# Performance work log

Measured on AMD Instinct MI355X. Metric: run time of the kernel, lower is better.

Reference implementation:

```python
import jax, jax.numpy as jnp
import numpy as np

FACTOR = 5

def setup_inputs() -> dict:
    key = jax.random.key(0)
    k1, k2, k3, k4 = jax.random.split(key, 4)
    B, L, H, D = 4, 2048, 8, 64
    sample_k = min(FACTOR * int(np.ceil(np.log(L))), L)  # 40
    return {
        "queries": jax.random.normal(k1, (B, L, H, D), dtype=jnp.float32),
        "keys": jax.random.normal(k2, (B, L, H, D), dtype=jnp.float32),
        "values": jax.random.normal(k3, (B, L, H, D), dtype=jnp.float32),
        "index_sample": jax.random.randint(k4, (L, sample_k), 0, L, dtype=jnp.int32),
    }

def reference(queries, keys, values, index_sample):
    # [B, L, H, D] -> [B, H, L, D]
    Q = jnp.transpose(queries, (0, 2, 1, 3))
    K = jnp.transpose(keys, (0, 2, 1, 3))
    V = jnp.transpose(values, (0, 2, 1, 3))
    B, H, L_Q, D = Q.shape
    L_K = K.shape[2]
    u = min(FACTOR * int(np.ceil(np.log(L_Q))), L_Q)  # n_top

    # --- _prob_QK: sampled QK scores ---
    # K_sample: [B, H, L_Q, sample_k, D]
    K_sample = K[:, :, index_sample, :]
    # Q_K_sample[b,h,l,s] = Q[b,h,l,:] . K_sample[b,h,l,s,:]
    Q_K_sample = jnp.einsum('bhld,bhlsd->bhls', Q, K_sample)
    # sparsity measure M: max - mean over L_K
    M = Q_K_sample.max(axis=-1) - Q_K_sample.sum(axis=-1) / L_K  # [B,H,L_Q]
    _, M_top = jax.lax.top_k(M, u)  # [B,H,u]

    # reduced Q -> full scores against all keys
    Q_reduce = jnp.take_along_axis(Q, M_top[..., None], axis=2)  # [B,H,u,D]
    scores = jnp.einsum('bhud,bhkd->bhuk', Q_reduce, K)  # [B,H,u,L_K]
    scale = 1.0 / jnp.sqrt(jnp.asarray(D, dtype=scores.dtype))
    scores = scores * scale

    # --- initial context: mean of V over keys (mask_flag=False) ---
    V_mean = V.mean(axis=-2)  # [B,H,D]
    context = jnp.broadcast_to(V_mean[:, :, None, :], (B, H, L_Q, D))

    # --- update context at top-u query positions ---
    attn = jax.nn.softmax(scores, axis=-1)  # [B,H,u,L_K]
    ctx_top = jnp.einsum('bhuk,bhkd->bhud', attn, V)  # [B,H,u,D]
    b_idx = jnp.arange(B)[:, None, None]
    h_idx = jnp.arange(H)[None, :, None]
    context = context.at[b_idx, h_idx, M_top].set(ctx_top)
    return context  # [B, H, L_Q, D]
```

## Files before the change

### kernel.cpp

```cpp
#include <hip/hip_runtime.h>
#include <math.h>

#define LL 2048
#define HH 8
#define DD 64
#define SK 40
#define UU 40
#define SCALE 0.125f


__global__ __launch_bounds__(512) void k_m(
    const float* __restrict__ Q, const float* __restrict__ K,
    const int* __restrict__ idxs, float* __restrict__ Mout)
{
  int bx = blockIdx.x;
  int xcd = bx & 7, slot = bx >> 3;
  int b = xcd >> 1;
  int l = ((xcd & 1) << 10) | slot;
  int t = threadIdx.x;
  int h = t >> 6, lane = t & 63;
  int sg = lane >> 2, dg = lane & 3;

  int kb = b << 20;
  int qoff = kb + (l << 9) + (h << 6) + (dg << 2);
  float4 qv[4];
#pragma unroll
  for (int i = 0; i < 4; ++i)
    qv[i] = *(const float4*)(Q + qoff + i * 16);

  const int* ip = idxs + l * SK;
  int kconst = kb + (h << 6) + (dg << 2);
  float mx = -INFINITY, sum = 0.f;

#pragma unroll
  for (int c = 0; c < 3; ++c) {
    int s = c * 16 + sg;
    float p = 0.f;
    if (s < SK) {
      int koff = kconst + (ip[s] << 9);
      const float* krow = K + koff;
#pragma unroll
      for (int i = 0; i < 4; ++i) {
        float4 kv = *(const float4*)(krow + i * 16);
        p += qv[i].x * kv.x + qv[i].y * kv.y + qv[i].z * kv.z + qv[i].w * kv.w;
      }
    }
    p += __shfl_xor(p, 1);
    p += __shfl_xor(p, 2);
    if (s < SK) { mx = fmaxf(mx, p); sum += p; }
  }
#pragma unroll
  for (int off = 4; off <= 32; off <<= 1) {
    mx = fmaxf(mx, __shfl_xor(mx, off));
    sum += __shfl_xor(sum, off);
  }
  if (lane == 0) Mout[((b * HH + h) << 11) + l] = mx - sum * (1.0f / (float)LL);
}

__global__ __launch_bounds__(256) void k_topk(
    const float* __restrict__ Mv, int* __restrict__ Mtop)
{
  __shared__ float sv[LL];
  __shared__ float wm[4];
  __shared__ int wi[4];
  int bh = blockIdx.x;
  int t = threadIdx.x, w = t >> 6, ln = t & 63;
  for (int i = t; i < LL; i += 256) sv[i] = Mv[bh * LL + i];
  __syncthreads();
  for (int r = 0; r < UU; ++r) {
    float bv = -INFINITY; int bi = 0;
#pragma unroll
    for (int j = 0; j < 8; ++j) {
      int i = t + (j << 8);
      float v = sv[i];
      if (v > bv) { bv = v; bi = i; }
    }
#pragma unroll
    for (int off = 1; off < 64; off <<= 1) {
      float ov = __shfl_xor(bv, off);
      int oi = __shfl_xor(bi, off);
      if (ov > bv || (ov == bv && oi < bi)) { bv = ov; bi = oi; }
    }
    if (ln == 0) { wm[w] = bv; wi[w] = bi; }
    __syncthreads();
    if (t == 0) {
      float Bv = wm[0]; int Bi = wi[0];
#pragma unroll
      for (int k = 1; k < 4; ++k)
        if (wm[k] > Bv || (wm[k] == Bv && wi[k] < Bi)) { Bv = wm[k]; Bi = wi[k]; }
      Mtop[bh * UU + r] = Bi;
      sv[Bi] = -INFINITY;
    }
    __syncthreads();
  }
}

__global__ __launch_bounds__(256) void k_vpart(
    const float* __restrict__ V, float* __restrict__ part)
{
  int blk = blockIdx.x;
  int bh = blk >> 3, c = blk & 7;
  int b = bh >> 3, h = bh & 7;
  int t = threadIdx.x, d = t & 63, w = t >> 6;
  int l0 = (c << 8) + (w << 6);
  int base = (b << 20) + (l0 << 9) + (h << 6) + d;
  float a0 = 0, a1 = 0, a2 = 0, a3 = 0;
  for (int j = 0; j < 64; j += 4) {
    a0 += V[base + ((j + 0) << 9)];
    a1 += V[base + ((j + 1) << 9)];
    a2 += V[base + ((j + 2) << 9)];
    a3 += V[base + ((j + 3) << 9)];
  }
  __shared__ float sm[4][64];
  sm[w][d] = a0 + a1 + a2 + a3;
  __syncthreads();
  if (t < 64) part[(blk << 6) + t] = sm[0][t] + sm[1][t] + sm[2][t] + sm[3][t];
}

__global__ __launch_bounds__(256) void k_fill(
    const float4* __restrict__ part4, float4* __restrict__ out4)
{
  int i = blockIdx.x * 256 + threadIdx.x;
  int bh = i >> 15;
  __shared__ float4 vm[16];
  if (threadIdx.x < 16) {
    int d4 = threadIdx.x;
    float4 s = {0, 0, 0, 0};
#pragma unroll
    for (int c = 0; c < 8; ++c) {
      float4 p = part4[((bh << 3) + c) * 16 + d4];
      s.x += p.x; s.y += p.y; s.z += p.z; s.w += p.w;
    }
    const float inv = 1.0f / (float)LL;
    s.x *= inv; s.y *= inv; s.z *= inv; s.w *= inv;
    vm[d4] = s;
  }
  __syncthreads();
  out4[i] = vm[i & 15];
}

__global__ __launch_bounds__(512) void k_attn2(
    const float* __restrict__ Q, const float* __restrict__ K,
    const float* __restrict__ V, const int* __restrict__ Mtop,
    float* __restrict__ pm, float* __restrict__ pl, float4* __restrict__ pO4)
{
  __shared__ float4 Ks4[1024];
  __shared__ float Ps[8][256];
  __shared__ float4 Os4[4][2][4][16];
  __shared__ int gqi[8];

  int bx = blockIdx.x;
  int ch = bx & 7;
  int slot = bx >> 3;
  int bh = slot / 5, rg = slot % 5;
  int b = bh >> 3, h = bh & 7;
  int t = threadIdx.x;
  int w = t >> 6, ln = t & 63;
  int l0 = ch << 8;

  if (t < 8) gqi[t] = Mtop[bh * UU + rg * 8 + t];
  __syncthreads();

  float4 qv[16];
  {
    const float4* qrow = (const float4*)Q + (((b << 11) + gqi[w]) << 7) + (h << 4);
#pragma unroll
    for (int i = 0; i < 16; ++i) qv[i] = qrow[i];
  }

  const float4* K4 = (const float4*)K;
  int kbase = (((b << 11) + l0) << 7) + (h << 4);
  int col0 = t >> 4, d40 = t & 15;
  int sw0 = col0 * 16 + (d40 ^ (col0 & 7));
  float4 g0 = K4[kbase + col0 * 128 + d40];
  float4 g1 = K4[kbase + (col0 + 32) * 128 + d40];

  float sc[4];
#pragma unroll
  for (int st = 0; st < 4; ++st) {
    __syncthreads();
    Ks4[sw0] = g0;
    Ks4[sw0 + 512] = g1;
    float4 n0, n1;
    if (st < 3) {
      int lr = (st + 1) * 64;
      n0 = K4[kbase + (lr + col0) * 128 + d40];
      n1 = K4[kbase + (lr + col0 + 32) * 128 + d40];
    }
    __syncthreads();
    float s = 0.f;
#pragma unroll
    for (int d4 = 0; d4 < 16; ++d4) {
      float4 kv = Ks4[ln * 16 + (d4 ^ (ln & 7))];
      s += qv[d4].x * kv.x + qv[d4].y * kv.y + qv[d4].z * kv.z + qv[d4].w * kv.w;
    }
    sc[st] = s * SCALE;
    g0 = n0; g1 = n1;
  }

  float m = fmaxf(fmaxf(sc[0], sc[1]), fmaxf(sc[2], sc[3]));
#pragma unroll
  for (int off = 1; off < 64; off <<= 1) m = fmaxf(m, __shfl_xor(m, off));
  float lsum = 0.f;
#pragma unroll
  for (int st = 0; st < 4; ++st) {
    float p = __expf(sc[st] - m);
    Ps[w][st * 64 + ln] = p;
    lsum += p;
  }
#pragma unroll
  for (int off = 1; off < 64; off <<= 1) lsum += __shfl_xor(lsum, off);
  if (ln == 0) {
    int prow = bh * UU + rg * 8 + w;
    pm[prow * 8 + ch] = m;
    pl[prow * 8 + ch] = lsum;
  }
  __syncthreads();

  int rw = w >> 2, cq = w & 3;
  int cg = ln >> 4, d4 = ln & 15;
  float4 o0 = {0,0,0,0}, o1 = {0,0,0,0}, o2 = {0,0,0,0}, o3 = {0,0,0,0};
  int vb = (((b << 11) + l0 + cq * 64) << 7) + (h << 4);
  const float4* V4 = (const float4*)V;
#pragma unroll
  for (int i = 0; i < 16; ++i) {
    int c = i * 4 + cg;
    float4 v4 = V4[vb + c * 128 + d4];
    float p0 = Ps[rw * 4 + 0][cq * 64 + c];
    float p1 = Ps[rw * 4 + 1][cq * 64 + c];
    float p2 = Ps[rw * 4 + 2][cq * 64 + c];
    float p3 = Ps[rw * 4 + 3][cq * 64 + c];
    o0.x += p0 * v4.x; o0.y += p0 * v4.y; o0.z += p0 * v4.z; o0.w += p0 * v4.w;
    o1.x += p1 * v4.x; o1.y += p1 * v4.y; o1.z += p1 * v4.z; o1.w += p1 * v4.w;
    o2.x += p2 * v4.x; o2.y += p2 * v4.y; o2.z += p2 * v4.z; o2.w += p2 * v4.w;
    o3.x += p3 * v4.x; o3.y += p3 * v4.y; o3.z += p3 * v4.z; o3.w += p3 * v4.w;
  }
#pragma unroll
  for (int off = 16; off <= 32; off <<= 1) {
    o0.x += __shfl_xor(o0.x, off); o0.y += __shfl_xor(o0.y, off);
    o0.z += __shfl_xor(o0.z, off); o0.w += __shfl_xor(o0.w, off);
    o1.x += __shfl_xor(o1.x, off); o1.y += __shfl_xor(o1.y, off);
    o1.z += __shfl_xor(o1.z, off); o1.w += __shfl_xor(o1.w, off);
    o2.x += __shfl_xor(o2.x, off); o2.y += __shfl_xor(o2.y, off);
    o2.z += __shfl_xor(o2.z, off); o2.w += __shfl_xor(o2.w, off);
    o3.x += __shfl_xor(o3.x, off); o3.y += __shfl_xor(o3.y, off);
    o3.z += __shfl_xor(o3.z, off); o3.w += __shfl_xor(o3.w, off);
  }
  if (cg == 0) {
    Os4[cq][rw][0][d4] = o0;
    Os4[cq][rw][1][d4] = o1;
    Os4[cq][rw][2][d4] = o2;
    Os4[cq][rw][3][d4] = o3;
  }
  __syncthreads();

  if (t < 128) {
    int r = t >> 4, dd = t & 15;
    float4 a = Os4[0][r >> 2][r & 3][dd];
    float4 bq = Os4[1][r >> 2][r & 3][dd];
    float4 cc = Os4[2][r >> 2][r & 3][dd];
    float4 dq = Os4[3][r >> 2][r & 3][dd];
    float4 s;
    s.x = a.x + bq.x + cc.x + dq.x;
    s.y = a.y + bq.y + cc.y + dq.y;
    s.z = a.z + bq.z + cc.z + dq.z;
    s.w = a.w + bq.w + cc.w + dq.w;
    int prow = bh * UU + rg * 8 + r;
    pO4[(prow * 8 + ch) * 16 + dd] = s;
  }
}

__global__ __launch_bounds__(256) void k_comb(
    const float* __restrict__ pm, const float* __restrict__ pl,
    const float* __restrict__ pO, const int* __restrict__ Mtop,
    float* __restrict__ out)
{
  int row = blockIdx.x * 4 + (threadIdx.x >> 6);
  int ln = threadIdx.x & 63;
  int bh = row / UU, r40 = row % UU;
  float mm[8];
#pragma unroll
  for (int c = 0; c < 8; ++c) mm[c] = pm[row * 8 + c];
  float ms = mm[0];
#pragma unroll
  for (int c = 1; c < 8; ++c) ms = fmaxf(ms, mm[c]);
  float wsum = 0.f, o = 0.f;
#pragma unroll
  for (int c = 0; c < 8; ++c) {
    float wc = __expf(mm[c] - ms);
    wsum += wc * pl[row * 8 + c];
    o += wc * pO[(row * 8 + c) * 64 + ln];
  }
  int gq = Mtop[bh * UU + r40];
  out[((bh * LL + gq) << 6) + ln] = o / wsum;
}

extern "C" void kernel_launch(void* const* d_in, const int* in_sizes, int n_in,
                              void* d_out, int out_size, void* d_ws, size_t ws_size,
                              hipStream_t stream)
{
  (void)in_sizes; (void)n_in; (void)out_size; (void)ws_size;
  const float* Q = (const float*)d_in[0];
  const float* K = (const float*)d_in[1];
  const float* V = (const float*)d_in[2];
  const int* idxs = (const int*)d_in[3];
  float* out = (float*)d_out;

  float* wsf = (float*)d_ws;
  float* M     = wsf;
  float* part  = wsf + 65536;
  int*   Mtop  = (int*)(wsf + 83968);
  float* pm    = wsf + 85248;
  float* pl    = wsf + 95488;
  float* pO    = wsf + 105728;

  k_m    <<<8192, 512, 0, stream>>>(Q, K, idxs, M);
  k_topk <<<32,   256, 0, stream>>>(M, Mtop);
  k_vpart<<<256,  256, 0, stream>>>(V, part);
  k_fill <<<4096, 256, 0, stream>>>((const float4*)part, (float4*)out);
  k_attn2<<<1280, 512, 0, stream>>>(Q, K, V, Mtop, pm, pl, (float4*)pO);
  k_comb <<<320,  256, 0, stream>>>(pm, pl, pO, Mtop, out);
}
```

Baseline: 215.7 us.

## Restructure sampled-QK kernel: one wave per query row, all heads per wave

The sparsity-measure kernel now gives each block 8 query rows, one per wavefront, with each wave covering all 8 heads using 8 lanes per head. The row's sample indices are staged in shared memory, and 8 key gathers are issued before any compute to expose more memory-level parallelism. Each gathered key row (all heads, 2KB) is read contiguously by a single wave, and the grid shrinks eightfold. This trades fewer blocks and extra register pressure for better coalescing and less index reloading.

```diff
diff --git a/kernel.cpp b/kernel.cpp
--- a/kernel.cpp
+++ b/kernel.cpp
@@ -9,52 +9,55 @@
 #define SCALE 0.125f
 
 
-__global__ __launch_bounds__(512) void k_m(
+__global__ __launch_bounds__(512, 4) void k_m(
     const float* __restrict__ Q, const float* __restrict__ K,
     const int* __restrict__ idxs, float* __restrict__ Mout)
 {
+  __shared__ int sidx[8 * SK];
   int bx = blockIdx.x;
   int xcd = bx & 7, slot = bx >> 3;
   int b = xcd >> 1;
-  int l = ((xcd & 1) << 10) | slot;
+  int l0 = ((xcd & 1) << 10) | (slot << 3);
   int t = threadIdx.x;
-  int h = t >> 6, lane = t & 63;
-  int sg = lane >> 2, dg = lane & 3;
-
-  int kb = b << 20;
-  int qoff = kb + (l << 9) + (h << 6) + (dg << 2);
-  float4 qv[4];
-#pragma unroll
-  for (int i = 0; i < 4; ++i)
-    qv[i] = *(const float4*)(Q + qoff + i * 16);
-
-  const int* ip = idxs + l * SK;
-  int kconst = kb + (h << 6) + (dg << 2);
+  int w = t >> 6, lane = t & 63;
+  int l = l0 + w;
+  int h = lane >> 3, dg = lane & 7;
+
+  if (t < 8 * SK) sidx[t] = idxs[l0 * SK + t];
+
+  const float4* Q4 = (const float4*)Q;
+  int qoff = (((b << 11) + l) << 7) + (h << 4) + (dg << 1);
+  float4 q0 = Q4[qoff], q1 = Q4[qoff + 1];
+
+  const float4* K4 = (const float4*)K;
+  int kbb = b << 18;
+  int klo = (h << 4) + (dg << 1);
+
+  __syncthreads();
+
   float mx = -INFINITY, sum = 0.f;
-
-#pragma unroll
-  for (int c = 0; c < 3; ++c) {
-    int s = c * 16 + sg;
-    float p = 0.f;
-    if (s < SK) {
-      int koff = kconst + (ip[s] << 9);
-      const float* krow = K + koff;
-#pragma unroll
-      for (int i = 0; i < 4; ++i) {
-        float4 kv = *(const float4*)(krow + i * 16);
-        p += qv[i].x * kv.x + qv[i].y * kv.y + qv[i].z * kv.z + qv[i].w * kv.w;
-      }
-    }
-    p += __shfl_xor(p, 1);
-    p += __shfl_xor(p, 2);
-    if (s < SK) { mx = fmaxf(mx, p); sum += p; }
-  }
-#pragma unroll
-  for (int off = 4; off <= 32; off <<= 1) {
-    mx = fmaxf(mx, __shfl_xor(mx, off));
-    sum += __shfl_xor(sum, off);
-  }
-  if (lane == 0) Mout[((b * HH + h) << 11) + l] = mx - sum * (1.0f / (float)LL);
+#pragma unroll
+  for (int s0 = 0; s0 < SK; s0 += 8) {
+    float4 ka[8], kc[8];
+#pragma unroll
+    for (int j = 0; j < 8; ++j) {
+      int idx = sidx[w * SK + s0 + j];
+      int off = kbb + (idx << 7) + klo;
+      ka[j] = K4[off];
+      kc[j] = K4[off + 1];
+    }
+#pragma unroll
+    for (int j = 0; j < 8; ++j) {
+      float p = q0.x * ka[j].x + q0.y * ka[j].y + q0.z * ka[j].z + q0.w * ka[j].w
+              + q1.x * kc[j].x + q1.y * kc[j].y + q1.z * kc[j].z + q1.w * kc[j].w;
+      p += __shfl_xor(p, 1);
+      p += __shfl_xor(p, 2);
+      p += __shfl_xor(p, 4);
+      mx = fmaxf(mx, p);
+      sum += p;
+    }
+  }
+  if (dg == 0) Mout[((b * HH + h) << 11) + l] = mx - sum * (1.0f / (float)LL);
 }
 
 __global__ __launch_bounds__(256) void k_topk(
@@ -314,7 +317,7 @@
   float* pl    = wsf + 95488;
   float* pO    = wsf + 105728;
 
-  k_m    <<<8192, 512, 0, stream>>>(Q, K, idxs, M);
+  k_m    <<<1024, 512, 0, stream>>>(Q, K, idxs, M);
   k_topk <<<32,   256, 0, stream>>>(M, Mtop);
   k_vpart<<<256,  256, 0, stream>>>(V, part);
   k_fill <<<4096, 256, 0, stream>>>((const float4*)part, (float4*)out);
```

After: 208.0 us. -3.6%, faster.
